# Optimization experiments

Hardware: AMD Instinct MI355X
Metric: run time of the kernel (lower is better)

## Reference

```python
import jax, jax.numpy as jnp
import numpy as np

IDIM = 128
ODIM = 128
G = 8          # deformable groups
KH = KW = 3
K = KH * KW


def conv3x3(x, w, b):
    # x: [B,C,H,W], w: [O,I,3,3], stride 1, pad 1
    y = jax.lax.conv_general_dilated(x, w, (1, 1), ((1, 1), (1, 1)),
                                     dimension_numbers=('NCHW', 'OIHW', 'NCHW'))
    return y + b[None, :, None, None]


def deform_conv_v2(x, offset, mask, w, b):
    # x: [B,C,H,W]; offset: [B,2*G*K,H,W]; mask: [B,G*K,H,W] (pre-sigmoid)
    B, C, H, W = x.shape
    Cg = C // G
    off = offset.reshape(B, G, 2 * K, H, W)
    dy = off[:, :, 0::2]            # [B,G,K,H,W]
    dx = off[:, :, 1::2]
    m = jax.nn.sigmoid(mask).reshape(B, G, K, H, W)

    ky, kx = jnp.meshgrid(jnp.arange(KH), jnp.arange(KW), indexing='ij')
    ky = ky.reshape(K).astype(x.dtype)
    kx = kx.reshape(K).astype(x.dtype)
    hh = jnp.arange(H, dtype=x.dtype)
    ww = jnp.arange(W, dtype=x.dtype)
    # sampling positions (stride 1, pad 1, dilation 1)
    py = dy + (ky[:, None, None] + hh[None, :, None] - 1.0)   # [B,G,K,H,W]
    px = dx + (kx[:, None, None] + ww[None, None, :] - 1.0)

    y0 = jnp.floor(py)
    x0 = jnp.floor(px)
    ly = py - y0
    lx = px - x0

    x_flat = x.reshape(B, G, Cg, H * W)

    def gather(yi, xi):
        valid = ((yi >= 0) & (yi < H) & (xi >= 0) & (xi < W)).astype(x.dtype)
        yc = jnp.clip(yi, 0, H - 1).astype(jnp.int32)
        xc = jnp.clip(xi, 0, W - 1).astype(jnp.int32)
        idx = (yc * W + xc).reshape(B, G, 1, K * H * W)
        v = jnp.take_along_axis(x_flat, jnp.broadcast_to(idx, (B, G, Cg, K * H * W)), axis=3)
        return v.reshape(B, G, Cg, K, H, W) * valid[:, :, None]

    # bilinear interpolation with zero padding, fused with modulation mask
    v = (gather(y0, x0) * ((1 - ly) * (1 - lx))[:, :, None]
         + gather(y0, x0 + 1) * ((1 - ly) * lx)[:, :, None]
         + gather(y0 + 1, x0) * (ly * (1 - lx))[:, :, None]
         + gather(y0 + 1, x0 + 1) * (ly * lx)[:, :, None])
    v = v * m[:, :, None]                                      # [B,G,Cg,K,H,W]

    wr = w.reshape(w.shape[0], G, Cg, K)
    out = jnp.einsum('bgckhw,ogck->bohw', v, wr)
    return out + b[None, :, None, None]


def setup_inputs() -> dict:
    key = jax.random.key(0)
    ks = jax.random.split(key, 12)
    B, H, W = 2, 96, 96
    s = 0.05
    return {
        'R1': jax.random.normal(ks[0], (B, IDIM, H, W), jnp.float32),
        'Q0': jax.random.normal(ks[1], (B, IDIM, H, W), jnp.float32),
        'w1': jax.random.normal(ks[2], (ODIM, IDIM, 3, 3), jnp.float32) * s,
        'b1': jax.random.normal(ks[3], (ODIM,), jnp.float32) * s,
        'w2': jax.random.normal(ks[4], (ODIM, ODIM, 3, 3), jnp.float32) * s,
        'b2': jax.random.normal(ks[5], (ODIM,), jnp.float32) * s,
        'w_om': jax.random.normal(ks[6], (G * 3 * K, ODIM, 3, 3), jnp.float32) * s,
        'b_om': jax.random.normal(ks[7], (G * 3 * K,), jnp.float32) * s,
        'w_dcn': jax.random.normal(ks[8], (ODIM, IDIM, 3, 3), jnp.float32) * s,
        'b_dcn': jax.random.normal(ks[9], (ODIM,), jnp.float32) * s,
        'w_rq': jax.random.normal(ks[10], (ODIM, 2 * ODIM, 3, 3), jnp.float32) * s,
        'b_rq': jax.random.normal(ks[11], (ODIM,), jnp.float32) * s,
    }


def reference(R1, Q0, w1, b1, w2, b2, w_om, b_om, w_dcn, b_dcn, w_rq, b_rq):
    off = jax.nn.relu(conv3x3(R1 - Q0, w1, b1))
    off = jax.nn.relu(conv3x3(off, w2, b2))
    om = conv3x3(off, w_om, b_om)                 # [B, 3*G*K, H, W]
    o1, o2, mask = jnp.split(om, 3, axis=1)
    offset = jnp.concatenate([o1, o2], axis=1)    # [B, 2*G*K, H, W]
    fea = jax.nn.relu(deform_conv_v2(R1, offset, mask, w_dcn, b_dcn))
    fused = jnp.concatenate([fea, Q0], axis=1)
    return jax.nn.relu(conv3x3(fused, w_rq, b_rq))
```

## Files before the change

kernel.cpp:

```cpp
#include <hip/hip_runtime.h>

#define HH 96
#define WW 96
#define HW 9216
#define NPIX 18432
#define OMC 216
#define PP 9604

typedef __attribute__((ext_vector_type(8))) short short8x;
typedef __attribute__((ext_vector_type(8))) unsigned short ushort8x;
typedef __attribute__((ext_vector_type(4))) float f32x4;

__device__ __forceinline__ f32x4 mfma16(short8x a, short8x b, f32x4 c) {
    return __builtin_amdgcn_mfma_f32_16x16x32_bf16(a, b, c, 0, 0, 0);
}
__device__ __forceinline__ unsigned short f2bf(float f) {
    unsigned int u = __float_as_uint(f);
    u = (u + 0x7FFFu + ((u >> 16) & 1u)) >> 16;
    return (unsigned short)u;
}
__device__ __forceinline__ float bf2f(unsigned short b) {
    return __uint_as_float((unsigned int)b << 16);
}
__device__ __forceinline__ void split2(float v, unsigned short& h, unsigned short& l) {
    h = f2bf(v);
    l = f2bf(v - bf2f(h));
}
__device__ __forceinline__ void gld_lds16(const unsigned short* src, unsigned short* dst) {
    __builtin_amdgcn_global_load_lds(
        (const __attribute__((address_space(1))) unsigned int*)src,
        (__attribute__((address_space(3))) unsigned int*)dst, 16, 0, 0);
}

__global__ __launch_bounds__(256) void zero_borders(
    unsigned short* __restrict__ diffb,
    unsigned short* __restrict__ t1,
    unsigned short* __restrict__ catb)
{
    int i = blockIdx.x * 256 + threadIdx.x;
    if (i >= 776) return;
    int b = i / 388, r = i % 388;
    int y, x;
    if      (r < 98)  { y = 0;          x = r; }
    else if (r < 196) { y = 97;         x = r - 98; }
    else if (r < 292) { y = r - 196 + 1; x = 0; }
    else              { y = r - 292 + 1; x = 97; }
    size_t P = (size_t)b * PP + (size_t)y * 98 + x;
    ushort8x z = {};
    #pragma unroll
    for (int c = 0; c < 32; ++c) *(ushort8x*)&diffb[P * 256 + c * 8] = z;
    #pragma unroll
    for (int c = 0; c < 32; ++c) *(ushort8x*)&t1[P * 256 + c * 8] = z;
    #pragma unroll
    for (int c = 0; c < 64; ++c) *(ushort8x*)&catb[P * 512 + c * 8] = z;
}

__global__ __launch_bounds__(256) void prep_acts(
    const float* __restrict__ R1, const float* __restrict__ Q0,
    unsigned short* __restrict__ r1b,
    unsigned short* __restrict__ diffb,
    unsigned short* __restrict__ cat)
{
    __shared__ float tR[128][64];
    __shared__ float tQ[128][64];
    int tid = threadIdx.x;
    int p0  = blockIdx.x * 64;
    int b   = p0 / HW;
    int rem0 = p0 % HW;

    for (int e = tid; e < 2048; e += 256) {
        int c = e >> 4, j = e & 15;
        size_t base = ((size_t)(b * 128 + c)) * HW + rem0;
        *(float4*)&tR[c][j * 4] = *(const float4*)(R1 + base + j * 4);
        *(float4*)&tQ[c][j * 4] = *(const float4*)(Q0 + base + j * 4);
    }
    __syncthreads();

    int p = tid & 63, half = tid >> 6;
    int c0 = half * 32;
    int pix = p0 + p;
    int rm = pix % HW, yy = rm / 96, xx = rm % 96;
    size_t P = (size_t)b * PP + (size_t)(yy + 1) * 98 + xx + 1;
    ushort8x rb[4], dh[4], dl[4], qh[4], ql[4];
    #pragma unroll
    for (int cc = 0; cc < 32; ++cc) {
        float r = tR[c0 + cc][p], q = tQ[c0 + cc][p];
        rb[cc >> 3][cc & 7] = f2bf(r);
        unsigned short h, l;
        split2(r - q, h, l); dh[cc >> 3][cc & 7] = h; dl[cc >> 3][cc & 7] = l;
        split2(q, h, l);     qh[cc >> 3][cc & 7] = h; ql[cc >> 3][cc & 7] = l;
    }
    #pragma unroll
    for (int i = 0; i < 4; ++i) {
        *(ushort8x*)&r1b[(size_t)pix * 128 + c0 + i * 8] = rb[i];
        *(ushort8x*)&diffb[P * 256 +       c0 + i * 8] = dh[i];
        *(ushort8x*)&diffb[P * 256 + 128 + c0 + i * 8] = dl[i];
        *(ushort8x*)&cat [P * 512 + 128 + c0 + i * 8] = qh[i];
        *(ushort8x*)&cat [P * 512 + 384 + c0 + i * 8] = ql[i];
    }
}

__global__ __launch_bounds__(256) void prep_w(
    const float* __restrict__ w1, const float* __restrict__ w2,
    const float* __restrict__ wom, const float* __restrict__ bom,
    const float* __restrict__ wrq, const float* __restrict__ wdcn,
    unsigned short* __restrict__ p1, unsigned short* __restrict__ p2,
    unsigned short* __restrict__ pom, unsigned short* __restrict__ prq,
    unsigned short* __restrict__ pdcn, float* __restrict__ bomp)
{
    int idx = blockIdx.x * 256 + threadIdx.x;
    unsigned short h, l;
    if (idx < 147456) {
        int t = idx / 16384, o = (idx >> 7) & 127, ci = idx & 127;
        int src = (o * 128 + ci) * 9 + t;
        split2(w1[src], h, l);  p1[idx] = h;  p1[idx + 147456] = l;
        split2(w2[src], h, l);  p2[idx] = h;  p2[idx + 147456] = l;
        int dd = o * 1152 + ((ci >> 4) * 9 + t) * 16 + (ci & 15);
        split2(wdcn[src], h, l); pdcn[dd] = h; pdcn[dd + 147456] = l;
    }
    if (idx < 294912) {
        {
            int t = idx / 32768, o = (idx >> 7) & 255, ci = idx & 127;
            float v = (o < OMC) ? wom[(o * 128 + ci) * 9 + t] : 0.f;
            split2(v, h, l); pom[idx] = h; pom[idx + 294912] = l;
        }
        {
            int t = idx / 32768, o = (idx >> 8) & 127, ci = idx & 255;
            split2(wrq[(o * 256 + ci) * 9 + t], h, l);
            prq[idx] = h; prq[idx + 294912] = l;
        }
    }
    if (idx < 256) bomp[idx] = (idx < OMC) ? bom[idx] : 0.f;
}

template<int CIN, int COUTP, int MODE, bool RELU>
__global__ __launch_bounds__(256, 2) void conv_mfma(
    const unsigned short* __restrict__ in,
    const unsigned short* __restrict__ wpk,
    const float* __restrict__ bias,
    void* __restrict__ outv)
{
    constexpr int NKC = CIN / 32;
    constexpr int NSTEP = 9 * NKC;
    const size_t WPLANE = (size_t)9 * COUTP * CIN;

    __shared__ __align__(16) unsigned short s_buf[2][3072 + 8192];

    int tid = threadIdx.x;
    int wid = tid >> 6, lane = tid & 63;
    int r = lane & 15, q = lane >> 4;
    int bid = blockIdx.x;
    int swz = (bid & 7) * 48 + (bid >> 3);
    int rowid = swz >> 1, half = swz & 1;
    int b = rowid / 96, y = rowid % 96;
    int x0 = half * 48;
    int nbase = blockIdx.y * 128;

    auto stage = [&](int buf, int step) {
        int t = step / NKC, kc = step - t * NKC;
        int dy = t / 3 - 1, dx = t % 3 - 1;
        unsigned short* sb = &s_buf[buf][0];
        {
            int j = tid;
            int m = j >> 7, pl = (j >> 6) & 1, L = j & 63;
            int px = m * 16 + (L & 15), qd = L >> 4;
            const unsigned short* src = in +
                ((size_t)b * PP + (size_t)(y + 1 + dy) * 98 + (x0 + 1 + dx + px)) * (2 * CIN)
                + pl * CIN + kc * 32 + qd * 8;
            gld_lds16(src, sb + (size_t)(wid * 64) * 8);
        }
        if (tid < 128) {
            int j = 256 + tid;
            int m = j >> 7, pl = (j >> 6) & 1, L = j & 63;
            int px = m * 16 + (L & 15), qd = L >> 4;
            const unsigned short* src = in +
                ((size_t)b * PP + (size_t)(y + 1 + dy) * 98 + (x0 + 1 + dx + px)) * (2 * CIN)
                + pl * CIN + kc * 32 + qd * 8;
            gld_lds16(src, sb + (size_t)(256 + wid * 64) * 8);
        }
        const unsigned short* wbase = wpk + ((size_t)t * COUTP + nbase) * CIN + kc * 32;
        #pragma unroll
        for (int c = 0; c < 4; ++c) {
            int j = c * 256 + tid;
            int ni = (j >> 7) & 1, pl = (j >> 6) & 1, L = j & 63;
            int rr = L & 15, qq = L >> 4;
            const unsigned short* src = wbase + (size_t)pl * WPLANE
                + (size_t)(c * 32 + ni * 16 + rr) * CIN + qq * 8;
            gld_lds16(src, sb + 3072 + (size_t)(c * 256 + wid * 64) * 8);
        }
    };

    f32x4 acc[3][2] = {};

    auto compute = [&](int buf) {
        const unsigned short* sb = &s_buf[buf][0];
        short8x AH[3], AL[3], BH[2], BL[2];
        #pragma unroll
        for (int m = 0; m < 3; ++m) {
            AH[m] = *(const short8x*)(sb + m * 1024 + lane * 8);
            AL[m] = *(const short8x*)(sb + m * 1024 + 512 + lane * 8);
        }
        #pragma unroll
        for (int n = 0; n < 2; ++n) {
            BH[n] = *(const short8x*)(sb + 3072 + wid * 2048 + n * 1024 + lane * 8);
            BL[n] = *(const short8x*)(sb + 3072 + wid * 2048 + n * 1024 + 512 + lane * 8);
        }
        #pragma unroll
        for (int m = 0; m < 3; ++m) {
            #pragma unroll
            for (int n = 0; n < 2; ++n) {
                acc[m][n] = mfma16(AH[m], BH[n], acc[m][n]);
                acc[m][n] = mfma16(AL[m], BH[n], acc[m][n]);
                acc[m][n] = mfma16(AH[m], BL[n], acc[m][n]);
            }
        }
    };

    stage(0, 0);
    __syncthreads();
    int cur = 0;
    for (int k = 0; k < NSTEP; ++k) {
        if (k + 1 < NSTEP) stage(cur ^ 1, k + 1);
        compute(cur);
        __syncthreads();
        cur ^= 1;
    }

    #pragma unroll
    for (int m = 0; m < 3; ++m) {
        #pragma unroll
        for (int n = 0; n < 2; ++n) {
            int o = nbase + wid * 32 + n * 16 + r;
            float bv = bias[o];
            #pragma unroll
            for (int j = 0; j < 4; ++j) {
                int px = m * 16 + q * 4 + j;
                int xx = x0 + px;
                float v = acc[m][n][j] + bv;
                if (RELU) v = fmaxf(v, 0.f);
                if (MODE == 0) {
                    size_t P = (size_t)b * PP + (size_t)(y + 1) * 98 + xx + 1;
                    unsigned short h, l; split2(v, h, l);
                    ((unsigned short*)outv)[P * 2 * COUTP + o] = h;
                    ((unsigned short*)outv)[P * 2 * COUTP + COUTP + o] = l;
                } else if (MODE == 1) {
                    if (o < OMC)
                        ((unsigned short*)outv)[((size_t)b * HW + y * 96 + xx) * OMC + o] = f2bf(v);
                } else {
                    ((float*)outv)[((size_t)b * 128 + o) * HW + y * 96 + xx] = v;
                }
            }
        }
    }
}

__global__ __launch_bounds__(256, 4) void deform_mfma(
    const unsigned short* __restrict__ xb,
    const unsigned short* __restrict__ omf,
    const unsigned short* __restrict__ wpk,
    const float* __restrict__ bias,
    unsigned short* __restrict__ cat)
{
    __shared__ __align__(16) unsigned short s_v[16][1160];

    int tid = threadIdx.x;
    int pix0 = blockIdx.x * 16;
    int b = pix0 / HW;

    for (int e = tid; e < 1152; e += 256) {
        int p = e & 15, gk = e >> 4;
        int pix = pix0 + p;
        int rem = pix % HW;
        int hh = rem / 96, ww = rem % 96;
        int g = gk / 9, k = gk % 9;
        const unsigned short* op = omf + (size_t)pix * OMC;
        float dy = bf2f(op[g * 18 + 2 * k]);
        float dx = bf2f(op[g * 18 + 2 * k + 1]);
        float mr = bf2f(op[144 + g * 9 + k]);
        float m = 1.f / (1.f + __expf(-mr));
        float py = dy + (float)(k / 3) + (float)hh - 1.f;
        float px = dx + (float)(k % 3) + (float)ww - 1.f;
        float fy = floorf(py), fx = floorf(px);
        int y0 = (int)fy, x0 = (int)fx;
        float ly = py - fy, lx = px - fx;
        float cw[4] = {(1.f - ly) * (1.f - lx), (1.f - ly) * lx,
                       ly * (1.f - lx), ly * lx};
        ushort8x cv0[4], cv1[4];
        #pragma unroll
        for (int j = 0; j < 4; ++j) {
            int yy = y0 + (j >> 1), xx = x0 + (j & 1);
            bool valid = (yy >= 0) && (yy < HH) && (xx >= 0) && (xx < WW);
            int yc = yy < 0 ? 0 : (yy > 95 ? 95 : yy);
            int xc = xx < 0 ? 0 : (xx > 95 ? 95 : xx);
            const unsigned short* cp =
                xb + ((size_t)(b * HW + yc * 96 + xc)) * 128 + g * 16;
            cv0[j] = *(const ushort8x*)cp;
            cv1[j] = *(const ushort8x*)(cp + 8);
            cw[j] = valid ? cw[j] * m : 0.f;
        }
        ushort8x o0, o1;
        #pragma unroll
        for (int i = 0; i < 8; ++i) {
            float v0 = cw[0] * bf2f(cv0[0][i]) + cw[1] * bf2f(cv0[1][i])
                     + cw[2] * bf2f(cv0[2][i]) + cw[3] * bf2f(cv0[3][i]);
            float v1 = cw[0] * bf2f(cv1[0][i]) + cw[1] * bf2f(cv1[1][i])
                     + cw[2] * bf2f(cv1[2][i]) + cw[3] * bf2f(cv1[3][i]);
            o0[i] = f2bf(v0);
            o1[i] = f2bf(v1);
        }
        *(ushort8x*)&s_v[p][gk * 16    ] = o0;
        *(ushort8x*)&s_v[p][gk * 16 + 8] = o1;
    }
    __syncthreads();

    int wid = tid >> 6, lane = tid & 63;
    int r = lane & 15, q = lane >> 4;
    int n0 = wid * 32;
    f32x4 acc0 = {}, acc1 = {};
    const unsigned short* wb = wpk + (size_t)(n0 + r) * 1152 + q * 8;
    #pragma unroll
    for (int kp = 0; kp < 18; ++kp) {
        const int k0 = kp * 2, k1 = k0 + 1;
        short8x a0 = *(const short8x*)&s_v[r][k0 * 32 + q * 8];
        short8x a1 = *(const short8x*)&s_v[r][k1 * 32 + q * 8];
        short8x w00 = *(const short8x*)(wb + k0 * 32);
        short8x w10 = *(const short8x*)(wb + (size_t)16 * 1152 + k0 * 32);
        short8x l00 = *(const short8x*)(wb + 147456 + k0 * 32);
        short8x l10 = *(const short8x*)(wb + 147456 + (size_t)16 * 1152 + k0 * 32);
        short8x w01 = *(const short8x*)(wb + k1 * 32);
        short8x w11 = *(const short8x*)(wb + (size_t)16 * 1152 + k1 * 32);
        short8x l01 = *(const short8x*)(wb + 147456 + k1 * 32);
        short8x l11 = *(const short8x*)(wb + 147456 + (size_t)16 * 1152 + k1 * 32);
        acc0 = mfma16(a0, w00, acc0);
        acc1 = mfma16(a0, w10, acc1);
        acc0 = mfma16(a0, l00, acc0);
        acc1 = mfma16(a0, l10, acc1);
        acc0 = mfma16(a1, w01, acc0);
        acc1 = mfma16(a1, w11, acc1);
        acc0 = mfma16(a1, l01, acc0);
        acc1 = mfma16(a1, l11, acc1);
    }
    #pragma unroll
    for (int ni = 0; ni < 2; ++ni) {
        f32x4 A = ni ? acc1 : acc0;
        int o = n0 + ni * 16 + r;
        float bv = bias[o];
        #pragma unroll
        for (int j = 0; j < 4; ++j) {
            int pixel = pix0 + q * 4 + j;
            int bb = pixel / HW, rm = pixel % HW;
            int yy = rm / 96, xx = rm % 96;
            size_t P = (size_t)bb * PP + (size_t)(yy + 1) * 98 + xx + 1;
            float v = fmaxf(A[j] + bv, 0.f);
            unsigned short h, l;
            split2(v, h, l);
            cat[P * 512 + o] = h;
            cat[P * 512 + 256 + o] = l;
        }
    }
}

extern "C" void kernel_launch(void* const* d_in, const int* in_sizes, int n_in,
                              void* d_out, int out_size, void* d_ws, size_t ws_size,
                              hipStream_t stream) {
    const float* R1    = (const float*)d_in[0];
    const float* Q0    = (const float*)d_in[1];
    const float* w1    = (const float*)d_in[2];
    const float* b1    = (const float*)d_in[3];
    const float* w2    = (const float*)d_in[4];
    const float* b2    = (const float*)d_in[5];
    const float* w_om  = (const float*)d_in[6];
    const float* b_om  = (const float*)d_in[7];
    const float* w_dcn = (const float*)d_in[8];
    const float* b_dcn = (const float*)d_in[9];
    const float* w_rq  = (const float*)d_in[10];
    const float* b_rq  = (const float*)d_in[11];
    float* outp = (float*)d_out;

    char* w = (char*)d_ws;
    unsigned short* r1b   = (unsigned short*)w; w += (size_t)NPIX * 128 * 2;
    unsigned short* diffb = (unsigned short*)w; w += (size_t)2 * PP * 256 * 2;
    unsigned short* t1    = (unsigned short*)w; w += (size_t)2 * PP * 256 * 2;
    unsigned short* catb  = (unsigned short*)w; w += (size_t)2 * PP * 512 * 2;
    unsigned short* p1    = (unsigned short*)w; w += 2 * 147456 * 2;
    unsigned short* p2    = (unsigned short*)w; w += 2 * 147456 * 2;
    unsigned short* pdcn  = (unsigned short*)w; w += 2 * 147456 * 2;
    unsigned short* pom   = (unsigned short*)w; w += 2 * 294912 * 2;
    unsigned short* prq   = (unsigned short*)w; w += 2 * 294912 * 2;
    float*          bomp  = (float*)w;          w += 256 * 4;
    unsigned short* t2    = diffb;
    unsigned short* omf   = t1;

    zero_borders<<<4, 256, 0, stream>>>(diffb, t1, catb);
    prep_acts<<<288, 256, 0, stream>>>(R1, Q0, r1b, diffb, catb);
    prep_w<<<1152, 256, 0, stream>>>(w1, w2, w_om, b_om, w_rq, w_dcn,
                                     p1, p2, pom, prq, pdcn, bomp);

    conv_mfma<128, 128, 0, true ><<<dim3(384, 1), 256, 0, stream>>>(diffb, p1, b1, t1);
    conv_mfma<128, 128, 0, true ><<<dim3(384, 1), 256, 0, stream>>>(t1,    p2, b2, t2);
    conv_mfma<128, 256, 1, false><<<dim3(384, 2), 256, 0, stream>>>(t2,   pom, bomp, omf);

    deform_mfma<<<1152, 256, 0, stream>>>(r1b, omf, pdcn, b_dcn, catb);

    conv_mfma<256, 128, 2, true ><<<dim3(384, 1), 256, 0, stream>>>(catb, prq, b_rq, outp);
}
```

Before: 413.1 us.

## Shrink conv pixel tiles to 32 and double deform block width

```diff
diff --git a/kernel.cpp b/kernel.cpp
--- a/kernel.cpp
+++ b/kernel.cpp
@@ -134,7 +134,7 @@
 }
 
 template<int CIN, int COUTP, int MODE, bool RELU>
-__global__ __launch_bounds__(256, 2) void conv_mfma(
+__global__ __launch_bounds__(256, 3) void conv_mfma(
     const unsigned short* __restrict__ in,
     const unsigned short* __restrict__ wpk,
     const float* __restrict__ bias,
@@ -144,16 +144,16 @@
     constexpr int NSTEP = 9 * NKC;
     const size_t WPLANE = (size_t)9 * COUTP * CIN;
 
-    __shared__ __align__(16) unsigned short s_buf[2][3072 + 8192];
+    __shared__ __align__(16) unsigned short s_buf[2][2048 + 8192];
 
     int tid = threadIdx.x;
     int wid = tid >> 6, lane = tid & 63;
     int r = lane & 15, q = lane >> 4;
     int bid = blockIdx.x;
-    int swz = (bid & 7) * 48 + (bid >> 3);
-    int rowid = swz >> 1, half = swz & 1;
-    int b = rowid / 96, y = rowid % 96;
-    int x0 = half * 48;
+    int swz = (bid & 7) * 72 + (bid >> 3);
+    int yg = swz / 3;
+    int b = yg / 96, y = yg % 96;
+    int x0 = (swz % 3) * 32;
     int nbase = blockIdx.y * 128;
 
     auto stage = [&](int buf, int step) {
@@ -161,52 +161,40 @@
         int dy = t / 3 - 1, dx = t % 3 - 1;
         unsigned short* sb = &s_buf[buf][0];
         {
-            int j = tid;
-            int m = j >> 7, pl = (j >> 6) & 1, L = j & 63;
-            int px = m * 16 + (L & 15), qd = L >> 4;
+            int m = wid >> 1, pl = wid & 1;
+            int px = m * 16 + r, qd = q;
             const unsigned short* src = in +
                 ((size_t)b * PP + (size_t)(y + 1 + dy) * 98 + (x0 + 1 + dx + px)) * (2 * CIN)
                 + pl * CIN + kc * 32 + qd * 8;
             gld_lds16(src, sb + (size_t)(wid * 64) * 8);
         }
-        if (tid < 128) {
-            int j = 256 + tid;
-            int m = j >> 7, pl = (j >> 6) & 1, L = j & 63;
-            int px = m * 16 + (L & 15), qd = L >> 4;
-            const unsigned short* src = in +
-                ((size_t)b * PP + (size_t)(y + 1 + dy) * 98 + (x0 + 1 + dx + px)) * (2 * CIN)
-                + pl * CIN + kc * 32 + qd * 8;
-            gld_lds16(src, sb + (size_t)(256 + wid * 64) * 8);
-        }
         const unsigned short* wbase = wpk + ((size_t)t * COUTP + nbase) * CIN + kc * 32;
         #pragma unroll
         for (int c = 0; c < 4; ++c) {
-            int j = c * 256 + tid;
-            int ni = (j >> 7) & 1, pl = (j >> 6) & 1, L = j & 63;
-            int rr = L & 15, qq = L >> 4;
+            int ni = (tid >> 7) & 1, pl = (tid >> 6) & 1;
             const unsigned short* src = wbase + (size_t)pl * WPLANE
-                + (size_t)(c * 32 + ni * 16 + rr) * CIN + qq * 8;
-            gld_lds16(src, sb + 3072 + (size_t)(c * 256 + wid * 64) * 8);
+                + (size_t)(c * 32 + ni * 16 + r) * CIN + q * 8;
+            gld_lds16(src, sb + 2048 + (size_t)(c * 256 + wid * 64) * 8);
         }
     };
 
-    f32x4 acc[3][2] = {};
+    f32x4 acc[2][2] = {};
 
     auto compute = [&](int buf) {
         const unsigned short* sb = &s_buf[buf][0];
-        short8x AH[3], AL[3], BH[2], BL[2];
-        #pragma unroll
-        for (int m = 0; m < 3; ++m) {
+        short8x AH[2], AL[2], BH[2], BL[2];
+        #pragma unroll
+        for (int m = 0; m < 2; ++m) {
             AH[m] = *(const short8x*)(sb + m * 1024 + lane * 8);
             AL[m] = *(const short8x*)(sb + m * 1024 + 512 + lane * 8);
         }
         #pragma unroll
         for (int n = 0; n < 2; ++n) {
-            BH[n] = *(const short8x*)(sb + 3072 + wid * 2048 + n * 1024 + lane * 8);
-            BL[n] = *(const short8x*)(sb + 3072 + wid * 2048 + n * 1024 + 512 + lane * 8);
-        }
-        #pragma unroll
-        for (int m = 0; m < 3; ++m) {
+            BH[n] = *(const short8x*)(sb + 2048 + wid * 2048 + n * 1024 + lane * 8);
+            BL[n] = *(const short8x*)(sb + 2048 + wid * 2048 + n * 1024 + 512 + lane * 8);
+        }
+        #pragma unroll
+        for (int m = 0; m < 2; ++m) {
             #pragma unroll
             for (int n = 0; n < 2; ++n) {
                 acc[m][n] = mfma16(AH[m], BH[n], acc[m][n]);
@@ -227,15 +215,14 @@
     }
 
     #pragma unroll
-    for (int m = 0; m < 3; ++m) {
+    for (int m = 0; m < 2; ++m) {
         #pragma unroll
         for (int n = 0; n < 2; ++n) {
             int o = nbase + wid * 32 + n * 16 + r;
             float bv = bias[o];
             #pragma unroll
             for (int j = 0; j < 4; ++j) {
-                int px = m * 16 + q * 4 + j;
-                int xx = x0 + px;
+                int xx = x0 + m * 16 + q * 4 + j;
                 float v = acc[m][n][j] + bv;
                 if (RELU) v = fmaxf(v, 0.f);
                 if (MODE == 0) {
@@ -254,7 +241,7 @@
     }
 }
 
-__global__ __launch_bounds__(256, 4) void deform_mfma(
+__global__ __launch_bounds__(512, 8) void deform_mfma(
     const unsigned short* __restrict__ xb,
     const unsigned short* __restrict__ omf,
     const unsigned short* __restrict__ wpk,
@@ -267,7 +254,7 @@
     int pix0 = blockIdx.x * 16;
     int b = pix0 / HW;
 
-    for (int e = tid; e < 1152; e += 256) {
+    for (int e = tid; e < 1152; e += 512) {
         int p = e & 15, gk = e >> 4;
         int pix = pix0 + p;
         int rem = pix % HW;
@@ -285,65 +272,67 @@
         float ly = py - fy, lx = px - fx;
         float cw[4] = {(1.f - ly) * (1.f - lx), (1.f - ly) * lx,
                        ly * (1.f - lx), ly * lx};
-        ushort8x cv0[4], cv1[4];
+        const unsigned short* cp[4];
         #pragma unroll
         for (int j = 0; j < 4; ++j) {
             int yy = y0 + (j >> 1), xx = x0 + (j & 1);
-            bool valid = (yy >= 0) && (yy < HH) && (xx >= 0) && (xx < WW);
-            int yc = yy < 0 ? 0 : (yy > 95 ? 95 : yy);
-            int xc = xx < 0 ? 0 : (xx > 95 ? 95 : xx);
-            const unsigned short* cp =
-                xb + ((size_t)(b * HW + yc * 96 + xc)) * 128 + g * 16;
-            cv0[j] = *(const ushort8x*)cp;
-            cv1[j] = *(const ushort8x*)(cp + 8);
+            bool valid = ((unsigned)yy < 96u) && ((unsigned)xx < 96u);
+            int yc = min(max(yy, 0), 95), xc = min(max(xx, 0), 95);
+            cp[j] = xb + ((size_t)(b * HW + yc * 96 + xc)) * 128 + g * 16;
             cw[j] = valid ? cw[j] * m : 0.f;
         }
-        ushort8x o0, o1;
-        #pragma unroll
-        for (int i = 0; i < 8; ++i) {
-            float v0 = cw[0] * bf2f(cv0[0][i]) + cw[1] * bf2f(cv0[1][i])
-                     + cw[2] * bf2f(cv0[2][i]) + cw[3] * bf2f(cv0[3][i]);
-            float v1 = cw[0] * bf2f(cv1[0][i]) + cw[1] * bf2f(cv1[1][i])
-                     + cw[2] * bf2f(cv1[2][i]) + cw[3] * bf2f(cv1[3][i]);
-            o0[i] = f2bf(v0);
-            o1[i] = f2bf(v1);
-        }
-        *(ushort8x*)&s_v[p][gk * 16    ] = o0;
-        *(ushort8x*)&s_v[p][gk * 16 + 8] = o1;
+        {
+            ushort8x c0 = *(const ushort8x*)cp[0];
+            ushort8x c1 = *(const ushort8x*)cp[1];
+            ushort8x c2 = *(const ushort8x*)cp[2];
+            ushort8x c3 = *(const ushort8x*)cp[3];
+            ushort8x o0;
+            #pragma unroll
+            for (int i = 0; i < 8; ++i) {
+                float v = cw[0] * bf2f(c0[i]) + cw[1] * bf2f(c1[i])
+                        + cw[2] * bf2f(c2[i]) + cw[3] * bf2f(c3[i]);
+                o0[i] = f2bf(v);
+            }
+            *(ushort8x*)&s_v[p][gk * 16] = o0;
+        }
+        {
+            ushort8x c0 = *(const ushort8x*)(cp[0] + 8);
+            ushort8x c1 = *(const ushort8x*)(cp[1] + 8);
+            ushort8x c2 = *(const ushort8x*)(cp[2] + 8);
+            ushort8x c3 = *(const ushort8x*)(cp[3] + 8);
+            ushort8x o1;
+            #pragma unroll
+            for (int i = 0; i < 8; ++i) {
+                float v = cw[0] * bf2f(c0[i]) + cw[1] * bf2f(c1[i])
+                        + cw[2] * bf2f(c2[i]) + cw[3] * bf2f(c3[i]);
+                o1[i] = f2bf(v);
+            }
+            *(ushort8x*)&s_v[p][gk * 16 + 8] = o1;
+        }
     }
     __syncthreads();
 
     int wid = tid >> 6, lane = tid & 63;
     int r = lane & 15, q = lane >> 4;
-    int n0 = wid * 32;
-    f32x4 acc0 = {}, acc1 = {};
+    int n0 = wid * 16;
+    f32x4 acc = {};
     const unsigned short* wb = wpk + (size_t)(n0 + r) * 1152 + q * 8;
     #pragma unroll
     for (int kp = 0; kp < 18; ++kp) {
         const int k0 = kp * 2, k1 = k0 + 1;
         short8x a0 = *(const short8x*)&s_v[r][k0 * 32 + q * 8];
         short8x a1 = *(const short8x*)&s_v[r][k1 * 32 + q * 8];
-        short8x w00 = *(const short8x*)(wb + k0 * 32);
-        short8x w10 = *(const short8x*)(wb + (size_t)16 * 1152 + k0 * 32);
-        short8x l00 = *(const short8x*)(wb + 147456 + k0 * 32);
-        short8x l10 = *(const short8x*)(wb + 147456 + (size_t)16 * 1152 + k0 * 32);
-        short8x w01 = *(const short8x*)(wb + k1 * 32);
-        short8x w11 = *(const short8x*)(wb + (size_t)16 * 1152 + k1 * 32);
-        short8x l01 = *(const short8x*)(wb + 147456 + k1 * 32);
-        short8x l11 = *(const short8x*)(wb + 147456 + (size_t)16 * 1152 + k1 * 32);
-        acc0 = mfma16(a0, w00, acc0);
-        acc1 = mfma16(a0, w10, acc1);
-        acc0 = mfma16(a0, l00, acc0);
-        acc1 = mfma16(a0, l10, acc1);
-        acc0 = mfma16(a1, w01, acc0);
-        acc1 = mfma16(a1, w11, acc1);
-        acc0 = mfma16(a1, l01, acc0);
-        acc1 = mfma16(a1, l11, acc1);
-    }
-    #pragma unroll
-    for (int ni = 0; ni < 2; ++ni) {
-        f32x4 A = ni ? acc1 : acc0;
-        int o = n0 + ni * 16 + r;
+        short8x wh0 = *(const short8x*)(wb + k0 * 32);
+        short8x wl0 = *(const short8x*)(wb + 147456 + k0 * 32);
+        short8x wh1 = *(const short8x*)(wb + k1 * 32);
+        short8x wl1 = *(const short8x*)(wb + 147456 + k1 * 32);
+        acc = mfma16(a0, wh0, acc);
+        acc = mfma16(a0, wl0, acc);
+        acc = mfma16(a1, wh1, acc);
+        acc = mfma16(a1, wl1, acc);
+    }
+    {
+        int o = n0 + r;
         float bv = bias[o];
         #pragma unroll
         for (int j = 0; j < 4; ++j) {
@@ -351,7 +340,7 @@
             int bb = pixel / HW, rm = pixel % HW;
             int yy = rm / 96, xx = rm % 96;
             size_t P = (size_t)bb * PP + (size_t)(yy + 1) * 98 + xx + 1;
-            float v = fmaxf(A[j] + bv, 0.f);
+            float v = fmaxf(acc[j] + bv, 0.f);
             unsigned short h, l;
             split2(v, h, l);
             cat[P * 512 + o] = h;
@@ -380,12 +369,12 @@
     char* w = (char*)d_ws;
     unsigned short* r1b   = (unsigned short*)w; w += (size_t)NPIX * 128 * 2;
     unsigned short* diffb = (unsigned short*)w; w += (size_t)2 * PP * 256 * 2;
+    unsigned short* p1    = (unsigned short*)w; w += 2 * 147456 * 2;
+    unsigned short* p2    = (unsigned short*)w; w += 2 * 147456 * 2;
+    unsigned short* pom   = (unsigned short*)w; w += 2 * 294912 * 2;
     unsigned short* t1    = (unsigned short*)w; w += (size_t)2 * PP * 256 * 2;
     unsigned short* catb  = (unsigned short*)w; w += (size_t)2 * PP * 512 * 2;
-    unsigned short* p1    = (unsigned short*)w; w += 2 * 147456 * 2;
-    unsigned short* p2    = (unsigned short*)w; w += 2 * 147456 * 2;
     unsigned short* pdcn  = (unsigned short*)w; w += 2 * 147456 * 2;
-    unsigned short* pom   = (unsigned short*)w; w += 2 * 294912 * 2;
     unsigned short* prq   = (unsigned short*)w; w += 2 * 294912 * 2;
     float*          bomp  = (float*)w;          w += 256 * 4;
     unsigned short* t2    = diffb;
@@ -396,11 +385,11 @@
     prep_w<<<1152, 256, 0, stream>>>(w1, w2, w_om, b_om, w_rq, w_dcn,
                                      p1, p2, pom, prq, pdcn, bomp);
 
-    conv_mfma<128, 128, 0, true ><<<dim3(384, 1), 256, 0, stream>>>(diffb, p1, b1, t1);
-    conv_mfma<128, 128, 0, true ><<<dim3(384, 1), 256, 0, stream>>>(t1,    p2, b2, t2);
-    conv_mfma<128, 256, 1, false><<<dim3(384, 2), 256, 0, stream>>>(t2,   pom, bomp, omf);
-
-    deform_mfma<<<1152, 256, 0, stream>>>(r1b, omf, pdcn, b_dcn, catb);
-
-    conv_mfma<256, 128, 2, true ><<<dim3(384, 1), 256, 0, stream>>>(catb, prq, b_rq, outp);
-}
+    conv_mfma<128, 128, 0, true ><<<dim3(576, 1), 256, 0, stream>>>(diffb, p1, b1, t1);
+    conv_mfma<128, 128, 0, true ><<<dim3(576, 1), 256, 0, stream>>>(t1,    p2, b2, t2);
+    conv_mfma<128, 256, 1, false><<<dim3(576, 2), 256, 0, stream>>>(t2,   pom, bomp, omf);
+
+    deform_mfma<<<1152, 512, 0, stream>>>(r1b, omf, pdcn, b_dcn, catb);
+
+    conv_mfma<256, 128, 2, true ><<<dim3(576, 1), 256, 0, stream>>>(catb, prq, b_rq, outp);
+}
```

After: 542.5 us. +31.3%, slower.
